# Optimization experiments

Measured on AMD Instinct MI355X. Metric: run time of the kernel, lower is better.

Reference implementation:

```python
import jax, jax.numpy as jnp
import numpy as np

DIM = 2048
NUM_HEADS = 16
HEAD_DIM = DIM // NUM_HEADS  # 128
LC = HEAD_DIM // 2           # 64 complex pairs per head
B, S = 2, 2048
EPS = 1e-6


def setup_inputs() -> dict:
    key = jax.random.key(0)
    ks = jax.random.split(key, 12)
    x = jax.random.normal(ks[0], (B, S, DIM), dtype=jnp.float32)
    # freqs: unit-modulus complex rotations stored as (cos, sin), shape [S,1,LC,2]
    theta = jax.random.uniform(ks[1], (S, 1, LC), dtype=jnp.float32) * (2.0 * np.pi)
    freqs = jnp.stack([jnp.cos(theta), jnp.sin(theta)], axis=-1)
    scale = 0.02
    wq = jax.random.normal(ks[2], (DIM, DIM), dtype=jnp.float32) * scale
    bq = jnp.zeros((DIM,), dtype=jnp.float32)
    wk = jax.random.normal(ks[3], (DIM, DIM), dtype=jnp.float32) * scale
    bk = jnp.zeros((DIM,), dtype=jnp.float32)
    wv = jax.random.normal(ks[4], (DIM, DIM), dtype=jnp.float32) * scale
    bv = jnp.zeros((DIM,), dtype=jnp.float32)
    wo = jax.random.normal(ks[5], (DIM, DIM), dtype=jnp.float32) * scale
    bo = jnp.zeros((DIM,), dtype=jnp.float32)
    gq = jnp.ones((DIM,), dtype=jnp.float32)   # RMSNorm weight for q
    gk = jnp.ones((DIM,), dtype=jnp.float32)   # RMSNorm weight for k
    return {"x": x, "freqs": freqs, "wq": wq, "bq": bq, "wk": wk, "bk": bk,
            "wv": wv, "bv": bv, "wo": wo, "bo": bo, "gq": gq, "gk": gk}


def _rms_norm(x, g):
    xf = x.astype(jnp.float32)
    y = xf * jax.lax.rsqrt(jnp.mean(xf * xf, axis=-1, keepdims=True) + EPS)
    return y.astype(x.dtype) * g


def _rope_apply(x, freqs):
    # x: [B,S,D] -> complex pairs [B,S,H,LC,2]; freqs: [S,1,LC,2] (cos,sin)
    b, s, _ = x.shape
    xp = x.astype(jnp.float32).reshape(b, s, NUM_HEADS, LC, 2)
    xr, xi = xp[..., 0], xp[..., 1]
    cr = freqs[None, :, :, :, 0]  # [1,S,1,LC]
    ci = freqs[None, :, :, :, 1]
    out_r = xr * cr - xi * ci
    out_i = xr * ci + xi * cr
    out = jnp.stack([out_r, out_i], axis=-1).reshape(b, s, DIM)
    return out.astype(x.dtype)


def _attention(q, k, v):
    # q,k,v: [B,S,D] -> multihead SDPA -> [B,S,D]
    b, s, _ = q.shape
    qh = q.reshape(b, s, NUM_HEADS, HEAD_DIM).transpose(0, 2, 1, 3)
    kh = k.reshape(b, s, NUM_HEADS, HEAD_DIM).transpose(0, 2, 1, 3)
    vh = v.reshape(b, s, NUM_HEADS, HEAD_DIM).transpose(0, 2, 1, 3)
    scale = 1.0 / np.sqrt(HEAD_DIM).astype(np.float32)
    scores = jnp.einsum('bhqd,bhkd->bhqk', qh, kh) * scale
    probs = jax.nn.softmax(scores, axis=-1)
    out = jnp.einsum('bhqk,bhkd->bhqd', probs, vh)
    return out.transpose(0, 2, 1, 3).reshape(b, s, DIM)


def reference(x, freqs, wq, bq, wk, bk, wv, bv, wo, bo, gq, gk):
    q = _rms_norm(x @ wq.T + bq, gq)
    k = _rms_norm(x @ wk.T + bk, gk)
    v = x @ wv.T + bv
    q = _rope_apply(q, freqs)
    k = _rope_apply(k, freqs)
    attn = _attention(q, k, v)
    return attn @ wo.T + bo
```

## Files before the change

### kernel.cpp

```cpp
#include <hip/hip_runtime.h>
#include <cstdint>

typedef __bf16 bf16;
typedef __bf16 bf16x8 __attribute__((ext_vector_type(8)));
typedef __bf16 bf16x4 __attribute__((ext_vector_type(4)));
typedef float f32x4 __attribute__((ext_vector_type(4)));

#define DIMN 2048
#define SEQ  2048
#define NH   16
#define HD   128

__device__ __forceinline__ void gld_lds16(const bf16* g, bf16* l) {
    __builtin_amdgcn_global_load_lds(
        (const __attribute__((address_space(1))) void*)g,
        (__attribute__((address_space(3))) void*)l,
        16, 0, 0);
}

__global__ __launch_bounds__(256) void cast_f32_bf16(const float* __restrict__ src,
                                                     bf16* __restrict__ dst, int n4) {
    int i = blockIdx.x * 256 + threadIdx.x;
    if (i < n4) {
        float4 v = ((const float4*)src)[i];
        bf16x4 o;
        o[0] = (bf16)v.x; o[1] = (bf16)v.y; o[2] = (bf16)v.z; o[3] = (bf16)v.w;
        ((bf16x4*)dst)[i] = o;
    }
}

__global__ __launch_bounds__(256) void cast_w4(
    const float* __restrict__ s0, const float* __restrict__ s1,
    const float* __restrict__ s2, const float* __restrict__ s3,
    bf16* __restrict__ d0, bf16* __restrict__ d1,
    bf16* __restrict__ d2, bf16* __restrict__ d3, int n4) {
    const float* src = s0; bf16* dst = d0;
    if (blockIdx.y == 1) { src = s1; dst = d1; }
    if (blockIdx.y == 2) { src = s2; dst = d2; }
    if (blockIdx.y == 3) { src = s3; dst = d3; }
    int i = blockIdx.x * 256 + threadIdx.x;
    if (i < n4) {
        float4 v = ((const float4*)src)[i];
        bf16x4 o;
        o[0] = (bf16)v.x; o[1] = (bf16)v.y; o[2] = (bf16)v.z; o[3] = (bf16)v.w;
        ((bf16x4*)dst)[i] = o;
    }
}

template<int OUT_F32>
__global__ __launch_bounds__(256) void gemm_bt(
    const bf16* __restrict__ A,
    const bf16* __restrict__ Bw0, const bf16* __restrict__ Bw1, const bf16* __restrict__ Bw2,
    const float* __restrict__ bias0, const float* __restrict__ bias1, const float* __restrict__ bias2,
    void* __restrict__ C0, void* __restrict__ C1, void* __restrict__ C2)
{
    const int K = DIMN, N = DIMN;
    const bf16* Bw = Bw0; const float* bias = bias0; void* Cout = C0;
    if (blockIdx.z == 1) { Bw = Bw1; bias = bias1; Cout = C1; }
    if (blockIdx.z == 2) { Bw = Bw2; bias = bias2; Cout = C2; }

    __shared__ __attribute__((aligned(16))) bf16 As[128 * 32];
    __shared__ __attribute__((aligned(16))) bf16 Bs[128 * 32];

    const int t    = threadIdx.x;
    const int lane = t & 63, wave = t >> 6;
    const int l15  = lane & 15, quad = lane >> 4;
    const int wm   = (wave >> 1) * 64, wn = (wave & 1) * 64;
    const long bm  = (long)blockIdx.y * 128;
    const long bn  = (long)blockIdx.x * 128;

    const int  srow = t >> 2;
    const int  sseg = (t & 3) ^ ((srow >> 1) & 3);
    const int  scol = sseg * 8;
    const bf16* ag0 = A  + (bm + srow) * (long)K + scol;
    const bf16* ag1 = A  + (bm + 64 + srow) * (long)K + scol;
    const bf16* bg0 = Bw + (bn + srow) * (long)K + scol;
    const bf16* bg1 = Bw + (bn + 64 + srow) * (long)K + scol;
    bf16* asd = As + t * 8;
    bf16* bsd = Bs + t * 8;

    const int sw = (quad ^ ((l15 >> 1) & 3)) * 8;

    f32x4 acc[4][4] = {};

    for (int k0 = 0; k0 < K; k0 += 32) {
        gld_lds16(ag0 + k0, asd);
        gld_lds16(ag1 + k0, asd + 2048);
        gld_lds16(bg0 + k0, bsd);
        gld_lds16(bg1 + k0, bsd + 2048);
        __syncthreads();

        bf16x8 af[4], bfr[4];
#pragma unroll
        for (int i = 0; i < 4; i++)
            af[i] = *(const bf16x8*)(As + (wm + i * 16 + l15) * 32 + sw);
#pragma unroll
        for (int j = 0; j < 4; j++)
            bfr[j] = *(const bf16x8*)(Bs + (wn + j * 16 + l15) * 32 + sw);
#pragma unroll
        for (int i = 0; i < 4; i++)
#pragma unroll
            for (int j = 0; j < 4; j++)
                acc[i][j] = __builtin_amdgcn_mfma_f32_16x16x32_bf16(af[i], bfr[j], acc[i][j], 0, 0, 0);
        __syncthreads();
    }

#pragma unroll
    for (int j = 0; j < 4; j++) {
        const long col = bn + wn + j * 16 + l15;
        const float bv = bias[col];
#pragma unroll
        for (int i = 0; i < 4; i++) {
            const long row0 = bm + wm + i * 16 + quad * 4;
#pragma unroll
            for (int r = 0; r < 4; r++) {
                float v = acc[i][j][r] + bv;
                if (OUT_F32) ((float*)Cout)[(row0 + r) * N + col] = v;
                else         ((bf16*)Cout)[(row0 + r) * N + col] = (bf16)v;
            }
        }
    }
}

__global__ __launch_bounds__(256) void rmsnorm_rope(
    bf16* __restrict__ q, bf16* __restrict__ k,
    const float* __restrict__ gq, const float* __restrict__ gk,
    const float* __restrict__ freqs)
{
    const int row = blockIdx.x;
    bf16* ptr = blockIdx.y ? k : q;
    const float* g = blockIdx.y ? gk : gq;
    const int s = row & (SEQ - 1);
    const int t = threadIdx.x;
    const int lane = t & 63, wave = t >> 6;

    bf16* base = ptr + (long)row * DIMN + t * 8;
    bf16x8 raw = *(const bf16x8*)base;
    float v[8]; float ss = 0.f;
#pragma unroll
    for (int j = 0; j < 8; j++) { v[j] = (float)raw[j]; ss += v[j] * v[j]; }
#pragma unroll
    for (int off = 32; off; off >>= 1) ss += __shfl_xor(ss, off, 64);
    __shared__ float red[4];
    if (lane == 0) red[wave] = ss;
    __syncthreads();
    float tot = red[0] + red[1] + red[2] + red[3];
    float rn = rsqrtf(tot * (1.0f / DIMN) + 1e-6f);

    const int e0 = t * 8;
    bf16x8 o;
#pragma unroll
    for (int pp = 0; pp < 4; pp++) {
        int e = e0 + pp * 2;
        float xr = v[pp * 2]     * rn * g[e];
        float xi = v[pp * 2 + 1] * rn * g[e + 1];
        int lc = (e >> 1) & 63;
        float cr = freqs[s * 128 + lc * 2];
        float ci = freqs[s * 128 + lc * 2 + 1];
        o[pp * 2]     = (bf16)(xr * cr - xi * ci);
        o[pp * 2 + 1] = (bf16)(xr * ci + xi * cr);
    }
    *(bf16x8*)base = o;
}

__global__ __launch_bounds__(256) void transpose_v(const bf16* __restrict__ vin,
                                                   bf16* __restrict__ vt)
{
    __shared__ float tile[64][65];
    const int b = blockIdx.z, st = blockIdx.x, ct = blockIdx.y;
    const int tx = threadIdx.x & 63, ty = threadIdx.x >> 6;
#pragma unroll
    for (int ii = 0; ii < 16; ii++) {
        int r = ii * 4 + ty;
        tile[r][tx] = (float)vin[((long)(b * SEQ + st * 64 + r)) * DIMN + ct * 64 + tx];
    }
    __syncthreads();
#pragma unroll
    for (int ii = 0; ii < 16; ii++) {
        int c = ii * 4 + ty;
        vt[((long)(b * DIMN + ct * 64 + c)) * SEQ + st * 64 + tx] = (bf16)tile[tx][c];
    }
}

__global__ __launch_bounds__(256, 2) void attention(
    const bf16* __restrict__ Q, const bf16* __restrict__ Kb,
    const bf16* __restrict__ Vt, bf16* __restrict__ O)
{
    __shared__ __attribute__((aligned(16))) bf16 Ksh[64 * 136];
    __shared__ __attribute__((aligned(16))) bf16 Vsh[128 * 72];
    __shared__ __attribute__((aligned(16))) bf16 Psh[4][32 * 72];

    const int t = threadIdx.x;
    const int lane = t & 63, wave = t >> 6;
    const int l15 = lane & 15, quad = lane >> 4;
    const int bh = blockIdx.y, b = bh >> 4, h = bh & 15;
    const int qt = blockIdx.x;
    const long qrow0 = (long)b * SEQ + qt * 128 + wave * 32;
    const bf16* qbase = Q  + qrow0 * DIMN + h * HD;
    const bf16* kbase = Kb + (long)b * SEQ * DIMN + h * HD;
    const bf16* vbase = Vt + (long)bh * HD * SEQ;

    bf16x8 qf[2][4];
#pragma unroll
    for (int i = 0; i < 2; i++)
#pragma unroll
        for (int kd = 0; kd < 4; kd++)
            qf[i][kd] = *(const bf16x8*)(qbase + (long)(i * 16 + l15) * DIMN + kd * 32 + quad * 8);

    f32x4 o_acc[2][8] = {};
    float L[2][4] = {};
    const float scale = 0.08838834764831845f;
    const int rkey = (l15 >> 2) & 3;

    for (int kt = 0; kt < 32; kt++) {
#pragma unroll
        for (int it = 0; it < 4; it++) {
            int fs = it * 256 + t;
            int kr = fs >> 4, ks = fs & 15;
            *(uint4*)(Ksh + kr * 136 + ks * 8) =
                *(const uint4*)(kbase + (long)(kt * 64 + kr) * DIMN + ks * 8);
            int dr = fs >> 3, vs = fs & 7;
            *(uint4*)(Vsh + dr * 72 + vs * 8) =
                *(const uint4*)(vbase + (long)dr * SEQ + kt * 64 + vs * 8);
        }
        __syncthreads();

        f32x4 sc[2][4] = {};
#pragma unroll
        for (int j = 0; j < 4; j++)
#pragma unroll
            for (int kd = 0; kd < 4; kd++) {
                bf16x8 bfr = *(const bf16x8*)(Ksh + (j * 16 + l15) * 136 + kd * 32 + quad * 8);
                sc[0][j] = __builtin_amdgcn_mfma_f32_16x16x32_bf16(qf[0][kd], bfr, sc[0][j], 0, 0, 0);
                sc[1][j] = __builtin_amdgcn_mfma_f32_16x16x32_bf16(qf[1][kd], bfr, sc[1][j], 0, 0, 0);
            }

#pragma unroll
        for (int i = 0; i < 2; i++) {
            float rsum[4] = {0.f, 0.f, 0.f, 0.f};
#pragma unroll
            for (int j = 0; j < 4; j++) {
                const int seg = 2 * j + (l15 >> 3);
                const int segS = seg ^ quad;
#pragma unroll
                for (int r = 0; r < 4; r++) {
                    float e = __expf(sc[i][j][r] * scale);
                    rsum[r] += e;
                    Psh[wave][(i * 16 + quad * 4 + r) * 72 + segS * 8 + (l15 & 7)] = (bf16)e;
                }
            }
#pragma unroll
            for (int r = 0; r < 4; r++) {
                float vv = rsum[r];
                vv += __shfl_xor(vv, 1, 64);
                vv += __shfl_xor(vv, 2, 64);
                vv += __shfl_xor(vv, 4, 64);
                vv += __shfl_xor(vv, 8, 64);
                L[i][r] += vv;
            }
        }

#pragma unroll
        for (int kd = 0; kd < 2; kd++) {
            bf16x8 pa[2];
            pa[0] = *(const bf16x8*)(Psh[wave] + (l15)      * 72 + ((kd * 4 + quad) ^ rkey) * 8);
            pa[1] = *(const bf16x8*)(Psh[wave] + (16 + l15) * 72 + ((kd * 4 + quad) ^ rkey) * 8);
#pragma unroll
            for (int dj = 0; dj < 8; dj++) {
                bf16x8 vfr = *(const bf16x8*)(Vsh + (dj * 16 + l15) * 72 + kd * 32 + quad * 8);
                o_acc[0][dj] = __builtin_amdgcn_mfma_f32_16x16x32_bf16(pa[0], vfr, o_acc[0][dj], 0, 0, 0);
                o_acc[1][dj] = __builtin_amdgcn_mfma_f32_16x16x32_bf16(pa[1], vfr, o_acc[1][dj], 0, 0, 0);
            }
        }
        __syncthreads();
    }

#pragma unroll
    for (int i = 0; i < 2; i++)
#pragma unroll
        for (int r = 0; r < 4; r++) {
            float inv = 1.0f / L[i][r];
            long orow = qrow0 + i * 16 + quad * 4 + r;
#pragma unroll
            for (int dj = 0; dj < 8; dj++)
                O[orow * DIMN + h * HD + dj * 16 + l15] = (bf16)(o_acc[i][dj][r] * inv);
        }
}

extern "C" void kernel_launch(void* const* d_in, const int* in_sizes, int n_in,
                              void* d_out, int out_size, void* d_ws, size_t ws_size,
                              hipStream_t stream) {
    const float* x     = (const float*)d_in[0];
    const float* freqs = (const float*)d_in[1];
    const float* wq    = (const float*)d_in[2];
    const float* bq    = (const float*)d_in[3];
    const float* wk    = (const float*)d_in[4];
    const float* bk    = (const float*)d_in[5];
    const float* wv    = (const float*)d_in[6];
    const float* bv    = (const float*)d_in[7];
    const float* wo    = (const float*)d_in[8];
    const float* bo    = (const float*)d_in[9];
    const float* gq    = (const float*)d_in[10];
    const float* gk    = (const float*)d_in[11];
    float* out = (float*)d_out;

    const size_t MAT  = (size_t)4096 * 2048 * 2;
    const size_t WMAT = (size_t)2048 * 2048 * 2;
    char* p = (char*)d_ws;
    bf16* xb  = (bf16*)p; p += MAT;
    bf16* wqb = (bf16*)p; p += WMAT;
    bf16* wkb = (bf16*)p; p += WMAT;
    bf16* wvb = (bf16*)p; p += WMAT;
    bf16* wob = (bf16*)p; p += WMAT;
    bf16* qb  = (bf16*)p; p += MAT;
    bf16* kb  = (bf16*)p; p += MAT;
    bf16* vb  = (bf16*)p; p += MAT;
    bf16* vt  = (bf16*)p; p += MAT;
    bf16* attn = qb;

    cast_f32_bf16<<<8192, 256, 0, stream>>>(x, xb, 2097152);
    cast_w4<<<dim3(4096, 4), 256, 0, stream>>>(wq, wk, wv, wo, wqb, wkb, wvb, wob, 1048576);

    gemm_bt<0><<<dim3(16, 32, 3), 256, 0, stream>>>(xb, wqb, wkb, wvb,
                                                    bq, bk, bv, qb, kb, vb);
    rmsnorm_rope<<<dim3(4096, 2), 256, 0, stream>>>(qb, kb, gq, gk, freqs);
    transpose_v<<<dim3(32, 32, 2), 256, 0, stream>>>(vb, vt);
    attention<<<dim3(16, 32), 256, 0, stream>>>(qb, kb, vt, attn);
    gemm_bt<1><<<dim3(16, 32, 1), 256, 0, stream>>>(attn, wob, wob, wob,
                                                    bo, bo, bo, out, out, out);
}
```

Before: 469.3 us.

## Deepen GEMM K-tile, use direct-to-LDS loads and transposed scores in attention

The GEMM K-step doubles from 32 to 64 with an XOR-swizzled LDS layout, halving the number of barrier pairs per output tile. Attention now loads K and V tiles with global_load_lds into swizzled, unpadded LDS, and computes transposed scores (K as the A operand), so probabilities are written as packed bf16x4 and row sums need fewer shuffles. The softmax scale is folded into Q during the RMSNorm/RoPE pass, removing a multiply per score. Costs include more LDS per GEMM block and an extra barrier plus shared-memory exchange for the row sums at the end; softmax still runs without max subtraction.

After: 411.1 us. 12.4% less time.

```diff
diff --git a/kernel.cpp b/kernel.cpp
--- a/kernel.cpp
+++ b/kernel.cpp
@@ -59,8 +59,8 @@
     if (blockIdx.z == 1) { Bw = Bw1; bias = bias1; Cout = C1; }
     if (blockIdx.z == 2) { Bw = Bw2; bias = bias2; Cout = C2; }
 
-    __shared__ __attribute__((aligned(16))) bf16 As[128 * 32];
-    __shared__ __attribute__((aligned(16))) bf16 Bs[128 * 32];
+    __shared__ __attribute__((aligned(16))) bf16 As[128 * 64];
+    __shared__ __attribute__((aligned(16))) bf16 Bs[128 * 64];
 
     const int t    = threadIdx.x;
     const int lane = t & 63, wave = t >> 6;
@@ -69,39 +69,45 @@
     const long bm  = (long)blockIdx.y * 128;
     const long bn  = (long)blockIdx.x * 128;
 
-    const int  srow = t >> 2;
-    const int  sseg = (t & 3) ^ ((srow >> 1) & 3);
-    const int  scol = sseg * 8;
-    const bf16* ag0 = A  + (bm + srow) * (long)K + scol;
-    const bf16* ag1 = A  + (bm + 64 + srow) * (long)K + scol;
-    const bf16* bg0 = Bw + (bn + srow) * (long)K + scol;
-    const bf16* bg1 = Bw + (bn + 64 + srow) * (long)K + scol;
-    bf16* asd = As + t * 8;
-    bf16* bsd = Bs + t * 8;
-
-    const int sw = (quad ^ ((l15 >> 1) & 3)) * 8;
+    const bf16* agp[4]; const bf16* bgp[4]; bf16* asd[4]; bf16* bsd[4];
+#pragma unroll
+    for (int it = 0; it < 4; it++) {
+        int fs  = it * 256 + t;
+        int row = fs >> 3;
+        int gs  = (fs & 7) ^ (row & 7);
+        agp[it] = A  + (bm + row) * (long)K + gs * 8;
+        bgp[it] = Bw + (bn + row) * (long)K + gs * 8;
+        asd[it] = As + fs * 8;
+        bsd[it] = Bs + fs * 8;
+    }
+    const int swl = l15 & 7;
 
     f32x4 acc[4][4] = {};
 
-    for (int k0 = 0; k0 < K; k0 += 32) {
-        gld_lds16(ag0 + k0, asd);
-        gld_lds16(ag1 + k0, asd + 2048);
-        gld_lds16(bg0 + k0, bsd);
-        gld_lds16(bg1 + k0, bsd + 2048);
+    for (int k0 = 0; k0 < K; k0 += 64) {
+#pragma unroll
+        for (int it = 0; it < 4; it++) {
+            gld_lds16(agp[it] + k0, asd[it]);
+            gld_lds16(bgp[it] + k0, bsd[it]);
+        }
         __syncthreads();
 
-        bf16x8 af[4], bfr[4];
-#pragma unroll
-        for (int i = 0; i < 4; i++)
-            af[i] = *(const bf16x8*)(As + (wm + i * 16 + l15) * 32 + sw);
-#pragma unroll
-        for (int j = 0; j < 4; j++)
-            bfr[j] = *(const bf16x8*)(Bs + (wn + j * 16 + l15) * 32 + sw);
-#pragma unroll
-        for (int i = 0; i < 4; i++)
+#pragma unroll
+        for (int ks2 = 0; ks2 < 2; ks2++) {
+            const int sw = ((ks2 * 4 + quad) ^ swl) * 8;
+            bf16x8 af[4], bfr[4];
+#pragma unroll
+            for (int i = 0; i < 4; i++)
+                af[i] = *(const bf16x8*)(As + (wm + i * 16 + l15) * 64 + sw);
 #pragma unroll
             for (int j = 0; j < 4; j++)
-                acc[i][j] = __builtin_amdgcn_mfma_f32_16x16x32_bf16(af[i], bfr[j], acc[i][j], 0, 0, 0);
+                bfr[j] = *(const bf16x8*)(Bs + (wn + j * 16 + l15) * 64 + sw);
+#pragma unroll
+            for (int i = 0; i < 4; i++)
+#pragma unroll
+                for (int j = 0; j < 4; j++)
+                    acc[i][j] = __builtin_amdgcn_mfma_f32_16x16x32_bf16(af[i], bfr[j], acc[i][j], 0, 0, 0);
+        }
         __syncthreads();
     }
 
@@ -130,6 +136,7 @@
     const int row = blockIdx.x;
     bf16* ptr = blockIdx.y ? k : q;
     const float* g = blockIdx.y ? gk : gq;
+    const float osc = blockIdx.y ? 1.0f : 0.08838834764831845f;
     const int s = row & (SEQ - 1);
     const int t = threadIdx.x;
     const int lane = t & 63, wave = t >> 6;
@@ -157,8 +164,8 @@
         int lc = (e >> 1) & 63;
         float cr = freqs[s * 128 + lc * 2];
         float ci = freqs[s * 128 + lc * 2 + 1];
-        o[pp * 2]     = (bf16)(xr * cr - xi * ci);
-        o[pp * 2 + 1] = (bf16)(xr * ci + xi * cr);
+        o[pp * 2]     = (bf16)((xr * cr - xi * ci) * osc);
+        o[pp * 2 + 1] = (bf16)((xr * ci + xi * cr) * osc);
     }
     *(bf16x8*)base = o;
 }
@@ -186,9 +193,10 @@
     const bf16* __restrict__ Q, const bf16* __restrict__ Kb,
     const bf16* __restrict__ Vt, bf16* __restrict__ O)
 {
-    __shared__ __attribute__((aligned(16))) bf16 Ksh[64 * 136];
-    __shared__ __attribute__((aligned(16))) bf16 Vsh[128 * 72];
+    __shared__ __attribute__((aligned(16))) bf16 Ksh[64 * 128];
+    __shared__ __attribute__((aligned(16))) bf16 Vsh[128 * 64];
     __shared__ __attribute__((aligned(16))) bf16 Psh[4][32 * 72];
+    __shared__ float Lsh[4][32];
 
     const int t = threadIdx.x;
     const int lane = t & 63, wave = t >> 6;
@@ -202,72 +210,71 @@
 
     bf16x8 qf[2][4];
 #pragma unroll
-    for (int i = 0; i < 2; i++)
+    for (int im = 0; im < 2; im++)
 #pragma unroll
         for (int kd = 0; kd < 4; kd++)
-            qf[i][kd] = *(const bf16x8*)(qbase + (long)(i * 16 + l15) * DIMN + kd * 32 + quad * 8);
+            qf[im][kd] = *(const bf16x8*)(qbase + (long)(im * 16 + l15) * DIMN + kd * 32 + quad * 8);
+
+    const bf16* kgp[4]; const bf16* vgp[4]; bf16* ksd[4]; bf16* vsd[4];
+#pragma unroll
+    for (int it = 0; it < 4; it++) {
+        int fs = it * 256 + t;
+        int kr = fs >> 4, kp = fs & 15, kks = kp ^ (kr & 15);
+        kgp[it] = kbase + (long)kr * DIMN + kks * 8;
+        ksd[it] = Ksh + fs * 8;
+        int dr = fs >> 3, vp = fs & 7, vks = vp ^ (dr & 7);
+        vgp[it] = vbase + (long)dr * SEQ + vks * 8;
+        vsd[it] = Vsh + fs * 8;
+    }
 
     f32x4 o_acc[2][8] = {};
-    float L[2][4] = {};
-    const float scale = 0.08838834764831845f;
-    const int rkey = (l15 >> 2) & 3;
+    float Lt[2] = {0.f, 0.f};
 
     for (int kt = 0; kt < 32; kt++) {
 #pragma unroll
         for (int it = 0; it < 4; it++) {
-            int fs = it * 256 + t;
-            int kr = fs >> 4, ks = fs & 15;
-            *(uint4*)(Ksh + kr * 136 + ks * 8) =
-                *(const uint4*)(kbase + (long)(kt * 64 + kr) * DIMN + ks * 8);
-            int dr = fs >> 3, vs = fs & 7;
-            *(uint4*)(Vsh + dr * 72 + vs * 8) =
-                *(const uint4*)(vbase + (long)dr * SEQ + kt * 64 + vs * 8);
+            gld_lds16(kgp[it] + (long)(kt * 64) * DIMN, ksd[it]);
+            gld_lds16(vgp[it] + kt * 64, vsd[it]);
         }
         __syncthreads();
 
-        f32x4 sc[2][4] = {};
-#pragma unroll
-        for (int j = 0; j < 4; j++)
+        f32x4 st[4][2] = {};
+#pragma unroll
+        for (int jk = 0; jk < 4; jk++)
 #pragma unroll
             for (int kd = 0; kd < 4; kd++) {
-                bf16x8 bfr = *(const bf16x8*)(Ksh + (j * 16 + l15) * 136 + kd * 32 + quad * 8);
-                sc[0][j] = __builtin_amdgcn_mfma_f32_16x16x32_bf16(qf[0][kd], bfr, sc[0][j], 0, 0, 0);
-                sc[1][j] = __builtin_amdgcn_mfma_f32_16x16x32_bf16(qf[1][kd], bfr, sc[1][j], 0, 0, 0);
+                bf16x8 kf = *(const bf16x8*)(Ksh + (jk * 16 + l15) * 128 + (((kd * 4 + quad) ^ l15) & 15) * 8);
+                st[jk][0] = __builtin_amdgcn_mfma_f32_16x16x32_bf16(kf, qf[0][kd], st[jk][0], 0, 0, 0);
+                st[jk][1] = __builtin_amdgcn_mfma_f32_16x16x32_bf16(kf, qf[1][kd], st[jk][1], 0, 0, 0);
             }
 
 #pragma unroll
-        for (int i = 0; i < 2; i++) {
-            float rsum[4] = {0.f, 0.f, 0.f, 0.f};
-#pragma unroll
-            for (int j = 0; j < 4; j++) {
-                const int seg = 2 * j + (l15 >> 3);
-                const int segS = seg ^ quad;
+        for (int im = 0; im < 2; im++) {
+            float part = 0.f;
+#pragma unroll
+            for (int jk = 0; jk < 4; jk++) {
+                bf16x4 pk;
 #pragma unroll
                 for (int r = 0; r < 4; r++) {
-                    float e = __expf(sc[i][j][r] * scale);
-                    rsum[r] += e;
-                    Psh[wave][(i * 16 + quad * 4 + r) * 72 + segS * 8 + (l15 & 7)] = (bf16)e;
+                    float e = __expf(st[jk][im][r]);
+                    part += e;
+                    pk[r] = (bf16)e;
                 }
+                *(bf16x4*)(Psh[wave] + (im * 16 + l15) * 72 + jk * 16 + quad * 4) = pk;
             }
-#pragma unroll
-            for (int r = 0; r < 4; r++) {
-                float vv = rsum[r];
-                vv += __shfl_xor(vv, 1, 64);
-                vv += __shfl_xor(vv, 2, 64);
-                vv += __shfl_xor(vv, 4, 64);
-                vv += __shfl_xor(vv, 8, 64);
-                L[i][r] += vv;
-            }
-        }
-
-#pragma unroll
-        for (int kd = 0; kd < 2; kd++) {
+            part += __shfl_xor(part, 16, 64);
+            part += __shfl_xor(part, 32, 64);
+            Lt[im] += part;
+        }
+
+#pragma unroll
+        for (int kd2 = 0; kd2 < 2; kd2++) {
             bf16x8 pa[2];
-            pa[0] = *(const bf16x8*)(Psh[wave] + (l15)      * 72 + ((kd * 4 + quad) ^ rkey) * 8);
-            pa[1] = *(const bf16x8*)(Psh[wave] + (16 + l15) * 72 + ((kd * 4 + quad) ^ rkey) * 8);
+            pa[0] = *(const bf16x8*)(Psh[wave] + (l15)      * 72 + kd2 * 32 + quad * 8);
+            pa[1] = *(const bf16x8*)(Psh[wave] + (16 + l15) * 72 + kd2 * 32 + quad * 8);
 #pragma unroll
             for (int dj = 0; dj < 8; dj++) {
-                bf16x8 vfr = *(const bf16x8*)(Vsh + (dj * 16 + l15) * 72 + kd * 32 + quad * 8);
+                bf16x8 vfr = *(const bf16x8*)(Vsh + (dj * 16 + l15) * 64 + (((kd2 * 4 + quad) ^ l15) & 7) * 8);
                 o_acc[0][dj] = __builtin_amdgcn_mfma_f32_16x16x32_bf16(pa[0], vfr, o_acc[0][dj], 0, 0, 0);
                 o_acc[1][dj] = __builtin_amdgcn_mfma_f32_16x16x32_bf16(pa[1], vfr, o_acc[1][dj], 0, 0, 0);
             }
@@ -275,11 +282,14 @@
         __syncthreads();
     }
 
+    if (quad == 0) { Lsh[wave][l15] = Lt[0]; Lsh[wave][16 + l15] = Lt[1]; }
+    __syncthreads();
+
 #pragma unroll
     for (int i = 0; i < 2; i++)
 #pragma unroll
         for (int r = 0; r < 4; r++) {
-            float inv = 1.0f / L[i][r];
+            float inv = 1.0f / Lsh[wave][i * 16 + quad * 4 + r];
             long orow = qrow0 + i * 16 + quad * 4 + r;
 #pragma unroll
             for (int dj = 0; dj < 8; dj++)
```
